# Optimization experiments

Hardware: AMD Instinct MI355X
Metric: run time of the kernel (lower is better)

The kernel has to match this reference:

```python
import jax, jax.numpy as jnp
import numpy as np
from jax import lax

LRELU_SLOPE = 0.2
LRELU_GAIN = float(np.sqrt(2.0))  # StyleGAN2 def_gain for lrelu


def setup_inputs() -> dict:
    key = jax.random.key(0)
    ks = jax.random.split(key, 6)
    B, Cin, Cout, R, W_DIM, K = 8, 128, 128, 256, 512, 3
    return {
        "x": jax.random.normal(ks[0], (B, Cin, R, R), dtype=jnp.float32),
        "w": jax.random.normal(ks[1], (B, W_DIM), dtype=jnp.float32),
        "affine_w": jax.random.normal(ks[2], (Cin, W_DIM), dtype=jnp.float32),
        "affine_b": jnp.ones((Cin,), dtype=jnp.float32),  # bias_init=1
        "weight": jax.random.normal(ks[3], (Cout, Cin, K, K), dtype=jnp.float32),
        "noise_const": jax.random.normal(ks[4], (R, R), dtype=jnp.float32),
        "noise_strength": jax.random.normal(ks[5], (1,), dtype=jnp.float32) * 0.1,
        "bias": jnp.zeros((Cout,), dtype=jnp.float32),
        "noise_mode": 1,  # 1 == 'const'
    }


def reference(x, w, affine_w, affine_b, weight, noise_const, noise_strength, bias, noise_mode):
    B, Cin, R, _ = x.shape
    w_dim = w.shape[1]
    # FullyConnectedLayer: runtime weight gain 1/sqrt(in_features), bias_init=1
    styles = w @ (affine_w * (1.0 / np.sqrt(w_dim))).T + affine_b  # [B, Cin]
    # modulated_conv2d with demodulation, expressed as input-scale / conv / output-scale
    # (exactly equivalent to materializing per-sample modulated+demodulated weights)
    x_mod = x * styles[:, :, None, None]
    y = lax.conv_general_dilated(
        x_mod, weight, window_strides=(1, 1), padding=[(1, 1), (1, 1)],
        dimension_numbers=("NCHW", "OIHW", "NCHW"))  # [B, Cout, R, R]
    # demod coeffs: rsqrt(sum_{i,kh,kw} (weight * style)^2)
    w2 = jnp.einsum("oihw,oihw->oi", weight, weight)            # [Cout, Cin]
    dcoef = lax.rsqrt(jnp.einsum("oi,bi->bo", w2, styles * styles) + 1e-8)  # [B, Cout]
    y = y * dcoef[:, :, None, None]
    # const noise, bias, lrelu, gain+clamp (gain=1)
    y = y + noise_const * noise_strength[0]
    y = y + bias[None, :, None, None]
    y = jnp.where(y >= 0, y, LRELU_SLOPE * y)
    return jnp.clip(y * LRELU_GAIN, -256.0, 256.0)
```

## Files before the change

### kernel.cpp

```cpp
#include <hip/hip_runtime.h>
#include <math.h>

typedef __bf16 bf8_t __attribute__((ext_vector_type(8)));
typedef short  s8_t  __attribute__((ext_vector_type(8)));
typedef float  f4_t  __attribute__((ext_vector_type(4)));

#define CIN   128
#define COUT  128
#define RES   256
#define WDIM  512
#define PROWS 258
#define PCOLS 264
#define PSTR  138
#define BGRP  (8 * PSTR)

static __device__ __forceinline__ unsigned short f2bf(float f) {
    unsigned u = __float_as_uint(f);
    unsigned r = (u + 0x7fffu + ((u >> 16) & 1u)) >> 16;
    return (unsigned short)r;
}

__global__ void k_styles(const float* __restrict__ w, const float* __restrict__ aw,
                         const float* __restrict__ ab, float* __restrict__ styles) {
    int t = blockIdx.x * 256 + threadIdx.x;
    int b = t >> 7, i = t & 127;
    const float4* wr = (const float4*)(w + b * WDIM);
    const float4* ar = (const float4*)(aw + i * WDIM);
    float s = 0.f;
    for (int j = 0; j < WDIM / 4; ++j) {
        float4 a = ar[j], c = wr[j];
        s += a.x * c.x + a.y * c.y + a.z * c.z + a.w * c.w;
    }
    styles[t] = s * 0.04419417382415922f + ab[i];
}

__global__ void k_wprep(const float* __restrict__ wt, float* __restrict__ w2,
                        unsigned short* __restrict__ wb2) {
    int t = blockIdx.x * 256 + threadIdx.x;
    int o = t >> 7, i = t & 127;
    int ks = i >> 5, c5 = i & 31;
    float s = 0.f;
    for (int kk = 0; kk < 9; ++kk) {
        float v = wt[(o * CIN + i) * 9 + kk];
        s += v * v;
        wb2[((kk * 4 + ks) * COUT + o) * 32 + c5] = f2bf(v);
    }
    w2[o * CIN + i] = s;
}

__global__ void k_dcoef(const float* __restrict__ w2, const float* __restrict__ styles,
                        float* __restrict__ dcoef) {
    int t = blockIdx.x * 256 + threadIdx.x;
    int b = t >> 7, o = t & 127;
    float s = 0.f;
    for (int i = 0; i < CIN; ++i) {
        float st = styles[b * CIN + i];
        s += w2[o * CIN + i] * st * st;
    }
    dcoef[t] = 1.0f / sqrtf(s + 1e-8f);
}

__global__ __launch_bounds__(256) void k_prep_x(
    const float* __restrict__ x, const float* __restrict__ styles,
    unsigned short* __restrict__ xb) {
    int t = blockIdx.x * 256 + threadIdx.x;
    int pc = t % PCOLS;
    int r1 = t / PCOLS;
    int pr = r1 % PROWS;
    int bc = r1 / PROWS;
    int b = bc >> 4, cig = bc & 15;
    int r = pr - 1, c = pc - 4;
    unsigned short v[8];
    if ((r >= 0) & (r < RES) & (c >= 0) & (c < RES)) {
        const float* xp = x + (((size_t)b * CIN + cig * 8) * RES + r) * RES + c;
        const float* st = styles + b * CIN + cig * 8;
        #pragma unroll
        for (int j = 0; j < 8; ++j)
            v[j] = f2bf(__builtin_nontemporal_load(xp + (size_t)j * RES * RES) * st[j]);
    } else {
        #pragma unroll
        for (int j = 0; j < 8; ++j) v[j] = 0;
    }
    *(s8_t*)(xb + (size_t)t * 8) = *(const s8_t*)v;
}

__global__ __launch_bounds__(512, 4) void k_conv18(
    const float* __restrict__ noise, const float* __restrict__ nstrp,
    const float* __restrict__ bias, const float* __restrict__ dcoef,
    const unsigned short* __restrict__ wb2, const unsigned short* __restrict__ xb,
    float* __restrict__ out) {

    __shared__ s8_t xs[2][BGRP];
    __shared__ float s_dc[COUT], s_bias[COUT];

    int blk0 = blockIdx.x;
    int blk  = (blk0 & 7) * 256 + (blk0 >> 3);
    int b   = blk >> 8;
    int rem = blk & 255;
    int y0  = (rem >> 1) << 1;
    int w0  = (rem & 1) << 7;

    int tid = threadIdx.x;
    int lane = tid & 63, wave = tid >> 6;
    int cq = wave & 3;
    int ri = wave >> 2;
    int mbase = cq * 32;
    int l15 = lane & 15, quad = lane >> 4;

    const unsigned short* xbb = xb + (size_t)b * ((size_t)16 * PROWS * PCOLS * 8);
    const unsigned short* awp = wb2 + (mbase + l15) * 32 + quad * 8;

    auto stage = [&](int slot, int p) {
        int pr = y0 + (p >> 1);
        int cb = (p & 1) * 8;
        #pragma unroll
        for (int li = 0; li < 3; ++li) {
            int l = wave + li * 8;
            if (l < 18) {
                int g = l * 64 + lane;
                if (g < BGRP) {
                    int cig = (int)(((unsigned)g * 30395u) >> 22);
                    int col = g - cig * PSTR;
                    int cs = col > 131 ? 131 : col;
                    const unsigned short* src = xbb
                        + (((size_t)(cb + cig) * PROWS + pr) * PCOLS + (w0 + 2 + cs)) * 8;
                    __builtin_amdgcn_global_load_lds(
                        (const __attribute__((address_space(1))) unsigned int*)src,
                        (__attribute__((address_space(3))) unsigned int*)&xs[slot][g],
                        16, 0, 0);
                }
            }
        }
    };

    f4_t acc[2][8];
    #pragma unroll
    for (int m = 0; m < 2; ++m)
        #pragma unroll
        for (int n = 0; n < 8; ++n)
            acc[m][n] = (f4_t)0.f;

    stage(0, 0);
    stage(1, 1);
    if (tid < 128)      s_dc[tid] = dcoef[b * COUT + tid];
    else if (tid < 256) s_bias[tid - 128] = bias[tid - 128];
    __syncthreads();

    #pragma unroll
    for (int p = 0; p < 8; ++p) {
        int buf = p & 1;
        int row = p >> 1, half = p & 1;
        int kh = row - ri;
        if (kh >= 0 && kh <= 2) {
            #pragma unroll
            for (int kw = 0; kw < 3; ++kw) {
                int kk = kh * 3 + kw;
                #pragma unroll
                for (int ks2 = 0; ks2 < 2; ++ks2) {
                    int ks = half * 2 + ks2;
                    const unsigned short* ak = awp + (kk * 4 + ks) * COUT * 32;
                    s8_t af[2];
                    #pragma unroll
                    for (int mt = 0; mt < 2; ++mt)
                        af[mt] = *(const s8_t*)(ak + mt * 16 * 32);
                    s8_t bfg[8];
                    #pragma unroll
                    for (int nt = 0; nt < 8; ++nt)
                        bfg[nt] = xs[buf][(ks2 * 4 + quad) * PSTR
                                          + nt * 16 + l15 + kw + 1];
                    __builtin_amdgcn_s_setprio(1);
                    #pragma unroll
                    for (int mt = 0; mt < 2; ++mt)
                        #pragma unroll
                        for (int nt = 0; nt < 8; ++nt)
                            acc[mt][nt] = __builtin_amdgcn_mfma_f32_16x16x32_bf16(
                                __builtin_bit_cast(bf8_t, af[mt]),
                                __builtin_bit_cast(bf8_t, bfg[nt]),
                                acc[mt][nt], 0, 0, 0);
                    __builtin_amdgcn_s_setprio(0);
                }
            }
        }
        __syncthreads();
        if (p + 2 < 8) stage(buf, p + 2);
    }

    float nstr = nstrp[0];
    int y = y0 + ri;
    const float* nrow = noise + y * RES + w0;
    float nz[8];
    #pragma unroll
    for (int nt = 0; nt < 8; ++nt)
        nz[nt] = nrow[nt * 16 + l15] * nstr;

    float* orow = out + (size_t)b * COUT * RES * RES + y * RES + w0;
    #pragma unroll
    for (int mt = 0; mt < 2; ++mt) {
        #pragma unroll
        for (int rg = 0; rg < 4; ++rg) {
            int co = mbase + mt * 16 + quad * 4 + rg;
            float dc = s_dc[co], bi = s_bias[co];
            #pragma unroll
            for (int nt = 0; nt < 8; ++nt) {
                int px = nt * 16 + l15;
                float v = acc[mt][nt][rg] * dc + nz[nt] + bi;
                v = (v >= 0.f) ? v : 0.2f * v;
                v *= 1.4142135623730951f;
                v = fminf(fmaxf(v, -256.f), 256.f);
                orow[(size_t)co * RES * RES + px] = v;
            }
        }
    }
}

__global__ __launch_bounds__(256) void k_conv_fb(
    const float* __restrict__ x, const float* __restrict__ noise,
    const float* __restrict__ nstrp, const float* __restrict__ bias,
    const float* __restrict__ styles, const float* __restrict__ dcoef,
    const unsigned short* __restrict__ wb2, float* __restrict__ out) {

    __shared__ s8_t xs[16 * 136];
    __shared__ float s_sty[CIN], s_dc[COUT], s_bias[COUT];

    int blk = blockIdx.x;
    int b   = blk >> 9;
    int rem = blk & 511;
    int h0  = rem >> 1;
    int w0  = (rem & 1) << 7;

    int tid = threadIdx.x;
    if (tid < 128) {
        s_sty[tid] = styles[b * CIN + tid];
    } else {
        s_dc[tid - 128]   = dcoef[b * COUT + tid - 128];
        s_bias[tid - 128] = bias[tid - 128];
    }

    int lane = tid & 63, wave = tid >> 6;
    int mbase = (wave & 1) * 64;
    int nbase = (wave >> 1) * 64;
    int l15 = lane & 15, quad = lane >> 4;

    f4_t acc[4][4];
    for (int m = 0; m < 4; ++m)
        for (int n = 0; n < 4; ++n)
            acc[m][n] = (f4_t)0.f;

    for (int kh = 0; kh < 3; ++kh) {
        int r = h0 - 1 + kh;
        bool rowok = (r >= 0) && (r < RES);
        int rc = rowok ? r : 0;
        const float* xrow = x + ((size_t)b * CIN * RES + rc) * RES;

        __syncthreads();
        for (int it = 0; it < 9; ++it) {
            int g = it * 256 + tid;
            if (g < 16 * 136) {
                int cig = g / 136, col = g - cig * 136;
                int wcol = w0 - 4 + col;
                bool ok = rowok && (wcol >= 0) && (wcol < RES);
                s8_t v8;
                for (int j = 0; j < 8; ++j) {
                    int ci = cig * 8 + j;
                    float v = ok ? xrow[(size_t)ci * RES * RES + wcol] * s_sty[ci] : 0.f;
                    v8[j] = (short)f2bf(v);
                }
                xs[g] = v8;
            }
        }
        __syncthreads();

        for (int kw = 0; kw < 3; ++kw) {
            int kk = kh * 3 + kw;
            for (int ks = 0; ks < 4; ++ks) {
                s8_t af[4], bfg[4];
                for (int mt = 0; mt < 4; ++mt) {
                    int co = mbase + mt * 16 + l15;
                    af[mt] = *(const s8_t*)(wb2 + ((kk * 4 + ks) * COUT + co) * 32
                                            + quad * 8);
                }
                int cig = ks * 4 + quad;
                for (int nt = 0; nt < 4; ++nt) {
                    int col = nbase + nt * 16 + l15 + kw + 3;
                    bfg[nt] = xs[cig * 136 + col];
                }
                for (int mt = 0; mt < 4; ++mt)
                    for (int nt = 0; nt < 4; ++nt)
                        acc[mt][nt] = __builtin_amdgcn_mfma_f32_16x16x32_bf16(
                            __builtin_bit_cast(bf8_t, af[mt]),
                            __builtin_bit_cast(bf8_t, bfg[nt]),
                            acc[mt][nt], 0, 0, 0);
            }
        }
    }

    float nstr = nstrp[0];
    const float* nrow = noise + h0 * RES + w0;
    float nz[4];
    for (int nt = 0; nt < 4; ++nt)
        nz[nt] = nrow[nbase + nt * 16 + l15] * nstr;

    float* orow = out + (size_t)b * COUT * RES * RES + h0 * RES + w0;
    for (int mt = 0; mt < 4; ++mt) {
        for (int rg = 0; rg < 4; ++rg) {
            int co = mbase + mt * 16 + quad * 4 + rg;
            float dc = s_dc[co], bi = s_bias[co];
            for (int nt = 0; nt < 4; ++nt) {
                int px = nbase + nt * 16 + l15;
                float v = acc[mt][nt][rg] * dc + nz[nt] + bi;
                v = (v >= 0.f) ? v : 0.2f * v;
                v *= 1.4142135623730951f;
                v = fminf(fmaxf(v, -256.f), 256.f);
                orow[(size_t)co * RES * RES + px] = v;
            }
        }
    }
}

extern "C" void kernel_launch(void* const* d_in, const int* in_sizes, int n_in,
                              void* d_out, int out_size, void* d_ws, size_t ws_size,
                              hipStream_t stream) {
    const float* x     = (const float*)d_in[0];
    const float* w     = (const float*)d_in[1];
    const float* aw    = (const float*)d_in[2];
    const float* ab    = (const float*)d_in[3];
    const float* wt    = (const float*)d_in[4];
    const float* noise = (const float*)d_in[5];
    const float* nstr  = (const float*)d_in[6];
    const float* bias  = (const float*)d_in[7];

    float* ws     = (float*)d_ws;
    float* styles = ws;
    float* dcoef  = ws + 1024;
    float* w2     = ws + 2048;
    unsigned short* wb2 = (unsigned short*)(ws + 2048 + 16384);
    const size_t xb_off   = 368640;
    const size_t xb_bytes = (size_t)8 * 16 * PROWS * PCOLS * 16;
    unsigned short* xb = (unsigned short*)((char*)d_ws + xb_off);
    float* out = (float*)d_out;

    hipLaunchKernelGGL(k_styles, dim3(4),  dim3(256), 0, stream, w, aw, ab, styles);
    hipLaunchKernelGGL(k_wprep,  dim3(64), dim3(256), 0, stream, wt, w2, wb2);
    hipLaunchKernelGGL(k_dcoef,  dim3(4),  dim3(256), 0, stream, w2, styles, dcoef);

    if (ws_size >= xb_off + xb_bytes) {
        hipLaunchKernelGGL(k_prep_x,  dim3(34056), dim3(256), 0, stream, x, styles, xb);
        hipLaunchKernelGGL(k_conv18,  dim3(2048),  dim3(512), 0, stream,
                           noise, nstr, bias, dcoef, wb2, xb, out);
    } else {
        hipLaunchKernelGGL(k_conv_fb, dim3(4096), dim3(256), 0, stream,
                           x, noise, nstr, bias, styles, dcoef, wb2, out);
    }
}
```

Baseline: 268.1 us.

## Switch conv inner loop to 32x32x16 bf16 MFMA with repacked weights

Replaces the 16x16x32 MFMA tiling with 32x32x16 MFMA tiles. Each wave now covers 64 output channels by 64 pixels instead of 32 by 128, so the weight layout is repacked into 16-channel k-slices and the LDS row stride changes from 138 to 135. The goal is fewer LDS fragment reads per MFMA and better operand reuse from the larger instruction shape, plus possibly fewer bank conflicts from the odd stride. The epilogue mapping and the fallback kernel's weight indexing are updated to match the new layout.

```diff
diff --git a/kernel.cpp b/kernel.cpp
--- a/kernel.cpp
+++ b/kernel.cpp
@@ -4,6 +4,7 @@
 typedef __bf16 bf8_t __attribute__((ext_vector_type(8)));
 typedef short  s8_t  __attribute__((ext_vector_type(8)));
 typedef float  f4_t  __attribute__((ext_vector_type(4)));
+typedef float  f16v  __attribute__((ext_vector_type(16)));
 
 #define CIN   128
 #define COUT  128
@@ -11,7 +12,7 @@
 #define WDIM  512
 #define PROWS 258
 #define PCOLS 264
-#define PSTR  138
+#define PSTR  135
 #define BGRP  (8 * PSTR)
 
 static __device__ __forceinline__ unsigned short f2bf(float f) {
@@ -35,15 +36,15 @@
 }
 
 __global__ void k_wprep(const float* __restrict__ wt, float* __restrict__ w2,
-                        unsigned short* __restrict__ wb2) {
+                        unsigned short* __restrict__ wb3) {
     int t = blockIdx.x * 256 + threadIdx.x;
     int o = t >> 7, i = t & 127;
-    int ks = i >> 5, c5 = i & 31;
+    int ks16 = i >> 4, i15 = i & 15;
     float s = 0.f;
     for (int kk = 0; kk < 9; ++kk) {
         float v = wt[(o * CIN + i) * 9 + kk];
         s += v * v;
-        wb2[((kk * 4 + ks) * COUT + o) * 32 + c5] = f2bf(v);
+        wb3[((kk * 8 + ks16) * COUT + o) * 16 + i15] = f2bf(v);
     }
     w2[o * CIN + i] = s;
 }
@@ -84,10 +85,10 @@
     *(s8_t*)(xb + (size_t)t * 8) = *(const s8_t*)v;
 }
 
-__global__ __launch_bounds__(512, 4) void k_conv18(
+__global__ __launch_bounds__(512, 4) void k_conv19(
     const float* __restrict__ noise, const float* __restrict__ nstrp,
     const float* __restrict__ bias, const float* __restrict__ dcoef,
-    const unsigned short* __restrict__ wb2, const unsigned short* __restrict__ xb,
+    const unsigned short* __restrict__ wb3, const unsigned short* __restrict__ xb,
     float* __restrict__ out) {
 
     __shared__ s8_t xs[2][BGRP];
@@ -102,13 +103,14 @@
 
     int tid = threadIdx.x;
     int lane = tid & 63, wave = tid >> 6;
-    int cq = wave & 3;
+    int ch = wave & 1;
+    int ph = (wave >> 1) & 1;
     int ri = wave >> 2;
-    int mbase = cq * 32;
-    int l15 = lane & 15, quad = lane >> 4;
+    int l31 = lane & 31, hi = lane >> 5;
 
     const unsigned short* xbb = xb + (size_t)b * ((size_t)16 * PROWS * PCOLS * 8);
-    const unsigned short* awp = wb2 + (mbase + l15) * 32 + quad * 8;
+    const unsigned short* awp3 = wb3 + (ch * 64 + l31) * 16 + hi * 8;
+    int pbase = ph * 64;
 
     auto stage = [&](int slot, int p) {
         int pr = y0 + (p >> 1);
@@ -116,10 +118,10 @@
         #pragma unroll
         for (int li = 0; li < 3; ++li) {
             int l = wave + li * 8;
-            if (l < 18) {
+            if (l < 17) {
                 int g = l * 64 + lane;
                 if (g < BGRP) {
-                    int cig = (int)(((unsigned)g * 30395u) >> 22);
+                    int cig = (int)(((unsigned)g * 31069u) >> 22);
                     int col = g - cig * PSTR;
                     int cs = col > 131 ? 131 : col;
                     const unsigned short* src = xbb
@@ -133,12 +135,12 @@
         }
     };
 
-    f4_t acc[2][8];
+    f16v acc[2][2];
     #pragma unroll
     for (int m = 0; m < 2; ++m)
         #pragma unroll
-        for (int n = 0; n < 8; ++n)
-            acc[m][n] = (f4_t)0.f;
+        for (int n = 0; n < 2; ++n)
+            acc[m][n] = (f16v)0.f;
 
     stage(0, 0);
     stage(1, 1);
@@ -156,24 +158,23 @@
             for (int kw = 0; kw < 3; ++kw) {
                 int kk = kh * 3 + kw;
                 #pragma unroll
-                for (int ks2 = 0; ks2 < 2; ++ks2) {
-                    int ks = half * 2 + ks2;
-                    const unsigned short* ak = awp + (kk * 4 + ks) * COUT * 32;
-                    s8_t af[2];
+                for (int k16 = 0; k16 < 4; ++k16) {
+                    int ks16 = half * 4 + k16;
+                    const unsigned short* ak = awp3 + (kk * 8 + ks16) * COUT * 16;
+                    s8_t af[2], bfg[2];
                     #pragma unroll
                     for (int mt = 0; mt < 2; ++mt)
-                        af[mt] = *(const s8_t*)(ak + mt * 16 * 32);
-                    s8_t bfg[8];
+                        af[mt] = *(const s8_t*)(ak + mt * 32 * 16);
                     #pragma unroll
-                    for (int nt = 0; nt < 8; ++nt)
-                        bfg[nt] = xs[buf][(ks2 * 4 + quad) * PSTR
-                                          + nt * 16 + l15 + kw + 1];
+                    for (int nt = 0; nt < 2; ++nt)
+                        bfg[nt] = xs[buf][(2 * k16 + hi) * PSTR
+                                          + pbase + nt * 32 + l31 + kw + 1];
                     __builtin_amdgcn_s_setprio(1);
                     #pragma unroll
                     for (int mt = 0; mt < 2; ++mt)
                         #pragma unroll
-                        for (int nt = 0; nt < 8; ++nt)
-                            acc[mt][nt] = __builtin_amdgcn_mfma_f32_16x16x32_bf16(
+                        for (int nt = 0; nt < 2; ++nt)
+                            acc[mt][nt] = __builtin_amdgcn_mfma_f32_32x32x16_bf16(
                                 __builtin_bit_cast(bf8_t, af[mt]),
                                 __builtin_bit_cast(bf8_t, bfg[nt]),
                                 acc[mt][nt], 0, 0, 0);
@@ -187,22 +188,22 @@
 
     float nstr = nstrp[0];
     int y = y0 + ri;
-    const float* nrow = noise + y * RES + w0;
-    float nz[8];
+    const float* nrow = noise + y * RES + w0 + pbase;
+    float nz[2];
     #pragma unroll
-    for (int nt = 0; nt < 8; ++nt)
-        nz[nt] = nrow[nt * 16 + l15] * nstr;
-
-    float* orow = out + (size_t)b * COUT * RES * RES + y * RES + w0;
+    for (int nt = 0; nt < 2; ++nt)
+        nz[nt] = nrow[nt * 32 + l31] * nstr;
+
+    float* orow = out + (size_t)b * COUT * RES * RES + y * RES + w0 + pbase;
     #pragma unroll
     for (int mt = 0; mt < 2; ++mt) {
         #pragma unroll
-        for (int rg = 0; rg < 4; ++rg) {
-            int co = mbase + mt * 16 + quad * 4 + rg;
+        for (int rg = 0; rg < 16; ++rg) {
+            int co = ch * 64 + mt * 32 + (rg & 3) + 8 * (rg >> 2) + 4 * hi;
             float dc = s_dc[co], bi = s_bias[co];
             #pragma unroll
-            for (int nt = 0; nt < 8; ++nt) {
-                int px = nt * 16 + l15;
+            for (int nt = 0; nt < 2; ++nt) {
+                int px = nt * 32 + l31;
                 float v = acc[mt][nt][rg] * dc + nz[nt] + bi;
                 v = (v >= 0.f) ? v : 0.2f * v;
                 v *= 1.4142135623730951f;
@@ -217,7 +218,7 @@
     const float* __restrict__ x, const float* __restrict__ noise,
     const float* __restrict__ nstrp, const float* __restrict__ bias,
     const float* __restrict__ styles, const float* __restrict__ dcoef,
-    const unsigned short* __restrict__ wb2, float* __restrict__ out) {
+    const unsigned short* __restrict__ wb3, float* __restrict__ out) {
 
     __shared__ s8_t xs[16 * 136];
     __shared__ float s_sty[CIN], s_dc[COUT], s_bias[COUT];
@@ -276,8 +277,9 @@
                 s8_t af[4], bfg[4];
                 for (int mt = 0; mt < 4; ++mt) {
                     int co = mbase + mt * 16 + l15;
-                    af[mt] = *(const s8_t*)(wb2 + ((kk * 4 + ks) * COUT + co) * 32
-                                            + quad * 8);
+                    af[mt] = *(const s8_t*)(wb3
+                        + ((kk * 8 + 2 * ks + (quad >> 1)) * COUT + co) * 16
+                        + (quad & 1) * 8);
                 }
                 int cig = ks * 4 + quad;
                 for (int nt = 0; nt < 4; ++nt) {
@@ -333,22 +335,22 @@
     float* styles = ws;
     float* dcoef  = ws + 1024;
     float* w2     = ws + 2048;
-    unsigned short* wb2 = (unsigned short*)(ws + 2048 + 16384);
+    unsigned short* wb3 = (unsigned short*)(ws + 2048 + 16384);
     const size_t xb_off   = 368640;
     const size_t xb_bytes = (size_t)8 * 16 * PROWS * PCOLS * 16;
     unsigned short* xb = (unsigned short*)((char*)d_ws + xb_off);
     float* out = (float*)d_out;
 
     hipLaunchKernelGGL(k_styles, dim3(4),  dim3(256), 0, stream, w, aw, ab, styles);
-    hipLaunchKernelGGL(k_wprep,  dim3(64), dim3(256), 0, stream, wt, w2, wb2);
+    hipLaunchKernelGGL(k_wprep,  dim3(64), dim3(256), 0, stream, wt, w2, wb3);
     hipLaunchKernelGGL(k_dcoef,  dim3(4),  dim3(256), 0, stream, w2, styles, dcoef);
 
     if (ws_size >= xb_off + xb_bytes) {
         hipLaunchKernelGGL(k_prep_x,  dim3(34056), dim3(256), 0, stream, x, styles, xb);
-        hipLaunchKernelGGL(k_conv18,  dim3(2048),  dim3(512), 0, stream,
-                           noise, nstr, bias, dcoef, wb2, xb, out);
+        hipLaunchKernelGGL(k_conv19,  dim3(2048),  dim3(512), 0, stream,
+                           noise, nstr, bias, dcoef, wb3, xb, out);
     } else {
         hipLaunchKernelGGL(k_conv_fb, dim3(4096), dim3(256), 0, stream,
-                           x, noise, nstr, bias, styles, dcoef, wb2, out);
-    }
-}
+                           x, noise, nstr, bias, styles, dcoef, wb3, out);
+    }
+}
```

New measurement: 304.5 us. 1.14x slower.
